# Performance work log

Hardware: AMD Instinct MI355X
Metric: run time of the kernel (lower is better)

Reference implementation:

```python
import jax, jax.numpy as jnp
import numpy as np

MAX_K = 16
CLUSTER_ITERS = 3
TEMP = 0.8
EPS = 1e-6


def setup_inputs() -> dict:
    key = jax.random.key(0)
    k1, k2 = jax.random.split(key, 2)
    B, C, H, W = 4, 256, 128, 128
    embeddings = jax.random.normal(k1, (B, C, H, W), dtype=jnp.float32)
    # 1x1 conv == per-pixel linear: weight [max_k, C], bias [max_k]
    seed_w = jax.random.normal(k2, (MAX_K, C), dtype=jnp.float32) * 0.05
    seed_b = jnp.zeros((MAX_K,), dtype=jnp.float32)
    return {"embeddings": embeddings, "seed_w": seed_w, "seed_b": seed_b, "k": 8}


def reference(embeddings, seed_w, seed_b, k):
    b, c, h, w = embeddings.shape
    n = h * w
    feats = embeddings.reshape(b, c, n)                     # [b,c,n]

    # seed_proj (1x1 conv) restricted to first k output channels
    seeds = jnp.einsum('oc,bcn->bon', seed_w[:k], feats) + seed_b[:k][None, :, None]
    assign = jax.nn.softmax(seeds, axis=1)                  # [b,k,n]
    proto = jnp.einsum('bkn,bcn->bkc', assign, feats) / (assign.sum(axis=2)[..., None] + EPS)

    # ||f||^2 is constant across iterations
    f_sq = jnp.sum(feats * feats, axis=1)                   # [b,n]

    logits = None
    for _ in range(CLUSTER_ITERS):                          # small fixed iter count
        p_sq = jnp.sum(proto * proto, axis=2)               # [b,k]
        cross = jnp.einsum('bkc,bcn->bkn', proto, feats)    # [b,k,n]
        # squared L2 distance via matmul trick (same math as (f-p)^2 sum over c)
        dist = f_sq[:, None, :] + p_sq[:, :, None] - 2.0 * cross
        logits = -dist / TEMP                               # [b,k,n]
        assign = jax.nn.softmax(logits, axis=1)
        denom = assign.sum(axis=2, keepdims=True) + EPS     # [b,k,1]
        proto = jnp.einsum('bkn,bcn->bkc', assign, feats) / denom

    logits_map = logits.reshape(b, k, h, w)
    probs = jax.nn.softmax(logits_map, axis=1)
    # bilinear upsample x4, align_corners=False (half-pixel) == jax 'linear' resize
    probs_full = jax.image.resize(probs, (b, k, 4 * h, 4 * w), method='linear')
    return probs_full, proto, logits_map
```

## Files before the change

### kernel.cpp

```cpp
#include <hip/hip_runtime.h>
#include <hip/hip_bf16.h>
#include <math.h>

#define BB   4
#define CCH  256
#define KK   8
#define NPIX 16384
#define TILE 64
#define NBLK 256
#define TEMP_INV 1.25f
#define EPSF 1e-6f

__device__ __forceinline__ float bf_lo(unsigned int u) { return __uint_as_float(u << 16); }
__device__ __forceinline__ float bf_hi(unsigned int u) { return __uint_as_float(u & 0xffff0000u); }

template<int MODE>
__global__ __launch_bounds__(512, 6)
void skm_pass(const float* __restrict__ feats,
              const float* __restrict__ seed_w,
              const float* __restrict__ seed_b,
              const float* __restrict__ proto_t,
              const float* __restrict__ psq_part,
              float* __restrict__ fsq,
              float* __restrict__ part_num,
              float* __restrict__ part_den,
              float* __restrict__ logits_out,
              float* __restrict__ probs_out)
{
    __shared__ unsigned int fb_s[CCH][32];
    __shared__ float cross_s[8][KK][66];
    __shared__ float w_s[KK][68];
    __shared__ float aux_s[8][TILE];

    const int t   = threadIdx.x;
    const int bid = blockIdx.x;
    const int b   = bid >> 8;
    const int blk = bid & 255;
    const int n0  = blk * TILE;

    const int p  = t & 63;
    const int g  = t >> 6;
    const int c0 = __builtin_amdgcn_readfirstlane(g) * 32;
    const float* fcol = feats + (size_t)b * CCH * NPIX + (size_t)c0 * NPIX + n0 + p;
    const float* pt   = proto_t + (size_t)b * CCH * KK + (size_t)c0 * KK;

    float cr[KK];
    #pragma unroll
    for (int k = 0; k < KK; ++k) cr[k] = 0.f;
    float fs = 0.f;

    #pragma unroll 8
    for (int cc = 0; cc < 32; ++cc) {
        const float f = fcol[(size_t)cc * NPIX];
        if (MODE == 0) fs = fmaf(f, f, fs);
        const int c  = c0 + cc;
        const int wp = (p >> 1) ^ ((c & 15) << 1);
        ((__hip_bfloat16*)fb_s)[(c << 6) + (wp << 1) + (p & 1)] = __float2bfloat16(f);
        if (MODE == 0) {
            #pragma unroll
            for (int k = 0; k < KK; ++k)
                cr[k] = fmaf(seed_w[k * CCH + c], f, cr[k]);
        } else {
            const float* pr = pt + cc * KK;
            #pragma unroll
            for (int k = 0; k < KK; ++k)
                cr[k] = fmaf(pr[k], f, cr[k]);
        }
    }
    #pragma unroll
    for (int k = 0; k < KK; ++k) cross_s[g][k][p] = cr[k];
    if (MODE == 0) aux_s[g][p] = fs;
    __syncthreads();

    {
        const int pp = t >> 3, k = t & 7;
        float lg = 0.f;
        #pragma unroll
        for (int gg = 0; gg < 8; ++gg) lg += cross_s[gg][k][pp];
        if (MODE == 0) {
            lg += seed_b[k];
            if (k == 0) {
                float fv = 0.f;
                #pragma unroll
                for (int gg = 0; gg < 8; ++gg) fv += aux_s[gg][pp];
                fsq[b * NPIX + n0 + pp] = fv;
            }
        } else {
            const float fv = fsq[b * NPIX + n0 + pp];
            const float4 q0 = ((const float4*)psq_part)[(b * KK + k) * 2];
            const float4 q1 = ((const float4*)psq_part)[(b * KK + k) * 2 + 1];
            const float pk = ((q0.x + q0.y) + (q0.z + q0.w))
                           + ((q1.x + q1.y) + (q1.z + q1.w));
            lg = (2.f * lg - fv - pk) * TEMP_INV;
        }
        float m = lg;
        m = fmaxf(m, __shfl_xor(m, 1, 64));
        m = fmaxf(m, __shfl_xor(m, 2, 64));
        m = fmaxf(m, __shfl_xor(m, 4, 64));
        const float e = expf(lg - m);
        float ssum = e;
        ssum += __shfl_xor(ssum, 1, 64);
        ssum += __shfl_xor(ssum, 2, 64);
        ssum += __shfl_xor(ssum, 4, 64);
        const float wv = e / ssum;
        w_s[k][pp] = wv;
        if (MODE == 2) aux_s[k][pp] = lg;
    }
    __syncthreads();

    if (MODE == 2) {
        const int k2 = t >> 6, p2 = t & 63;
        logits_out[((size_t)b * KK + k2) * NPIX + n0 + p2] = aux_s[k2][p2];
        probs_out [((size_t)b * KK + k2) * NPIX + n0 + p2] = w_s[k2][p2];
    }

    if (t < 256) {
        const int kk = t >> 5, ll = t & 31;
        float s = w_s[kk][2 * ll] + w_s[kk][2 * ll + 1];
        s += __shfl_xor(s, 16, 64);
        s += __shfl_xor(s, 8, 64);
        s += __shfl_xor(s, 4, 64);
        s += __shfl_xor(s, 2, 64);
        s += __shfl_xor(s, 1, 64);
        if (ll == 0) part_den[(b * NBLK + blk) * KK + kk] = s;
    }

    {
        const int c = t & 255, h = t >> 8;
        const int s2 = (c & 15) << 1;
        const uint2* row2 = (const uint2*)fb_s[c];
        float acc[KK];
        #pragma unroll
        for (int k = 0; k < KK; ++k) acc[k] = 0.f;
        #pragma unroll
        for (int j = 0; j < 8; ++j) {
            const uint2 u = row2[((16 * h + 2 * j) ^ s2) >> 1];
            const float f0 = bf_lo(u.x), f1 = bf_hi(u.x);
            const float f2 = bf_lo(u.y), f3 = bf_hi(u.y);
            const int px = 32 * h + 4 * j;
            #pragma unroll
            for (int k = 0; k < KK; ++k) {
                const float4 w4 = *(const float4*)&w_s[k][px];
                acc[k] = fmaf(f3, w4.w, fmaf(f2, w4.z,
                         fmaf(f1, w4.y, fmaf(f0, w4.x, acc[k]))));
            }
        }
        float (*acc_s)[KK][CCH] = (float (*)[KK][CCH])cross_s;
        #pragma unroll
        for (int k = 0; k < KK; ++k) acc_s[h][k][c] = acc[k];
        __syncthreads();
        #pragma unroll
        for (int u2 = t; u2 < KK * CCH; u2 += 512) {
            const int k = u2 >> 8, c2 = u2 & 255;
            part_num[(((size_t)b * NBLK + blk) * KK + k) * CCH + c2] =
                acc_s[0][k][c2] + acc_s[1][k][c2];
        }
    }
}

template<bool FINAL>
__global__ __launch_bounds__(256)
void skm_reduce(const float* __restrict__ part_num,
                const float* __restrict__ part_den,
                float* __restrict__ proto_t,
                float* __restrict__ psq_part,
                float* __restrict__ proto_out,
                const float* __restrict__ probs_ws,
                float* __restrict__ probs_full)
{
    const int bid = blockIdx.x;
    if (FINAL && bid >= 256) {
        const int gid = (bid - 256) * 256 + threadIdx.x;
        const int jb = gid & 127;
        const int i  = (gid >> 7) & 511;
        const int bk = gid >> 16;
        const float* src = probs_ws + (size_t)bk * NPIX;
        const float y   = i * 0.25f - 0.375f;
        const float y0f = floorf(y);
        const float fy  = y - y0f;
        const int   y0  = (int)y0f;
        const int ya = min(max(y0, 0), 127);
        const int yb = min(max(y0 + 1, 0), 127);
        const int xm = max(jb - 1, 0);
        const int xp = min(jb + 1, 127);
        const float* r0 = src + ya * 128;
        const float* r1 = src + yb * 128;
        const float wy0 = 1.f - fy;
        const float am = r0[xm] * wy0 + r1[xm] * fy;
        const float ac = r0[jb] * wy0 + r1[jb] * fy;
        const float ap = r0[xp] * wy0 + r1[xp] * fy;
        float4 o;
        o.x = 0.375f * am + 0.625f * ac;
        o.y = 0.125f * am + 0.875f * ac;
        o.z = 0.875f * ac + 0.125f * ap;
        o.w = 0.625f * ac + 0.375f * ap;
        ((float4*)probs_full)[gid] = o;
        return;
    }

    const int cq = bid & 7;
    const int bk = bid >> 3;
    const int b = bk >> 3, k = bk & 7;
    const int t = threadIdx.x;

    __shared__ float red[8][32];
    __shared__ float den_s[4];

    float dv = part_den[(b * NBLK + t) * KK + k];
    dv += __shfl_xor(dv, 32, 64);
    dv += __shfl_xor(dv, 16, 64);
    dv += __shfl_xor(dv, 8, 64);
    dv += __shfl_xor(dv, 4, 64);
    dv += __shfl_xor(dv, 2, 64);
    dv += __shfl_xor(dv, 1, 64);
    if ((t & 63) == 0) den_s[t >> 6] = dv;

    const int jj = t >> 5, cl = t & 31;
    const int c = cq * 32 + cl;
    float s = 0.f;
    #pragma unroll 4
    for (int j = 0; j < 32; ++j)
        s += part_num[(((size_t)b * NBLK + jj * 32 + j) * KK + k) * CCH + c];
    red[jj][cl] = s;
    __syncthreads();

    if (t < 32) {
        const float den = den_s[0] + den_s[1] + den_s[2] + den_s[3] + EPSF;
        float pv = 0.f;
        #pragma unroll
        for (int j2 = 0; j2 < 8; ++j2) pv += red[j2][t];
        pv /= den;
        const int c2 = cq * 32 + t;
        proto_t[((size_t)b * CCH + c2) * KK + k] = pv;
        if (proto_out) proto_out[(b * KK + k) * CCH + c2] = pv;
        float q = pv * pv;
        q += __shfl_xor(q, 16, 64);
        q += __shfl_xor(q, 8, 64);
        q += __shfl_xor(q, 4, 64);
        q += __shfl_xor(q, 2, 64);
        q += __shfl_xor(q, 1, 64);
        if (t == 0) psq_part[(b * KK + k) * 8 + cq] = q;
    }
}

extern "C" void kernel_launch(void* const* d_in, const int* in_sizes, int n_in,
                              void* d_out, int out_size, void* d_ws, size_t ws_size,
                              hipStream_t stream)
{
    const float* feats  = (const float*)d_in[0];
    const float* seed_w = (const float*)d_in[1];
    const float* seed_b = (const float*)d_in[2];

    float* out        = (float*)d_out;
    float* probs_full = out;
    float* proto_out  = out + 8388608;
    float* logits_out = out + 8388608 + 8192;

    float* ws       = (float*)d_ws;
    float* fsq      = ws;
    float* part_den = ws + 65536;
    float* proto_t  = part_den + 8192;
    float* psq_part = proto_t + 8192;
    float* probs_ws = psq_part + 256;
    float* part_num = probs_ws + 524288;

    const dim3 pg(BB * NBLK), pb(512);
    const dim3 rg(256), rb(256);

    skm_pass<0><<<pg, pb, 0, stream>>>(feats, seed_w, seed_b, proto_t, psq_part,
                                       fsq, part_num, part_den, nullptr, nullptr);
    skm_reduce<false><<<rg, rb, 0, stream>>>(part_num, part_den, proto_t, psq_part,
                                             nullptr, probs_ws, probs_full);
    skm_pass<1><<<pg, pb, 0, stream>>>(feats, seed_w, seed_b, proto_t, psq_part,
                                       fsq, part_num, part_den, nullptr, nullptr);
    skm_reduce<false><<<rg, rb, 0, stream>>>(part_num, part_den, proto_t, psq_part,
                                             nullptr, probs_ws, probs_full);
    skm_pass<1><<<pg, pb, 0, stream>>>(feats, seed_w, seed_b, proto_t, psq_part,
                                       fsq, part_num, part_den, nullptr, nullptr);
    skm_reduce<false><<<rg, rb, 0, stream>>>(part_num, part_den, proto_t, psq_part,
                                             nullptr, probs_ws, probs_full);
    skm_pass<2><<<pg, pb, 0, stream>>>(feats, seed_w, seed_b, proto_t, psq_part,
                                       fsq, part_num, part_den, logits_out, probs_ws);
    skm_reduce<true><<<dim3(256 + 8192), rb, 0, stream>>>(part_num, part_den, proto_t, psq_part,
                                                          proto_out, probs_ws, probs_full);
}
```

Baseline: 102.0 us.

## Cache bf16-packed features in first pass and reuse in later passes

The first pass now writes a bf16 copy of the features, two channels packed per 32-bit word, into workspace. Later passes read this packed copy instead of the fp32 input, which halves the feature bytes they load. The cost is an extra write pass of 32MB in pass 0. Later passes also compute the cross term from bf16-rounded values rather than fp32, which lowers accuracy.

```diff
diff --git a/kernel.cpp b/kernel.cpp
--- a/kernel.cpp
+++ b/kernel.cpp
@@ -13,6 +13,10 @@
 
 __device__ __forceinline__ float bf_lo(unsigned int u) { return __uint_as_float(u << 16); }
 __device__ __forceinline__ float bf_hi(unsigned int u) { return __uint_as_float(u & 0xffff0000u); }
+__device__ __forceinline__ unsigned short bfbits(float f) {
+    __hip_bfloat16 h = __float2bfloat16(f);
+    return *reinterpret_cast<unsigned short*>(&h);
+}
 
 template<int MODE>
 __global__ __launch_bounds__(512, 6)
@@ -25,7 +29,8 @@
               float* __restrict__ part_num,
               float* __restrict__ part_den,
               float* __restrict__ logits_out,
-              float* __restrict__ probs_out)
+              float* __restrict__ probs_out,
+              unsigned int* __restrict__ feats_pk)
 {
     __shared__ unsigned int fb_s[CCH][32];
     __shared__ float cross_s[8][KK][66];
@@ -41,35 +46,56 @@
     const int p  = t & 63;
     const int g  = t >> 6;
     const int c0 = __builtin_amdgcn_readfirstlane(g) * 32;
-    const float* fcol = feats + (size_t)b * CCH * NPIX + (size_t)c0 * NPIX + n0 + p;
-    const float* pt   = proto_t + (size_t)b * CCH * KK + (size_t)c0 * KK;
+    const float* pt = proto_t + (size_t)b * CCH * KK + (size_t)c0 * KK;
 
     float cr[KK];
     #pragma unroll
     for (int k = 0; k < KK; ++k) cr[k] = 0.f;
-    float fs = 0.f;
-
-    #pragma unroll 8
-    for (int cc = 0; cc < 32; ++cc) {
-        const float f = fcol[(size_t)cc * NPIX];
-        if (MODE == 0) fs = fmaf(f, f, fs);
-        const int c  = c0 + cc;
-        const int wp = (p >> 1) ^ ((c & 15) << 1);
-        ((__hip_bfloat16*)fb_s)[(c << 6) + (wp << 1) + (p & 1)] = __float2bfloat16(f);
-        if (MODE == 0) {
+
+    if (MODE == 0) {
+        const float* fcol = feats + (size_t)b * CCH * NPIX + (size_t)c0 * NPIX + n0 + p;
+        unsigned int* pkcol = feats_pk + (size_t)(b * 128 + (c0 >> 1)) * NPIX + n0 + p;
+        float fs = 0.f;
+        unsigned int pkbuf = 0;
+        #pragma unroll 8
+        for (int cc = 0; cc < 32; ++cc) {
+            const float f = fcol[(size_t)cc * NPIX];
+            fs = fmaf(f, f, fs);
+            const int c  = c0 + cc;
+            const int wp = (p >> 1) ^ ((c & 15) << 1);
+            const unsigned short hb = bfbits(f);
+            ((unsigned short*)fb_s)[(c << 6) + (wp << 1) + (p & 1)] = hb;
+            if ((cc & 1) == 0) pkbuf = hb;
+            else pkcol[(size_t)(cc >> 1) * NPIX] = pkbuf | ((unsigned int)hb << 16);
             #pragma unroll
             for (int k = 0; k < KK; ++k)
                 cr[k] = fmaf(seed_w[k * CCH + c], f, cr[k]);
-        } else {
-            const float* pr = pt + cc * KK;
+        }
+        aux_s[g][p] = fs;
+    } else {
+        const unsigned int* pkcol = feats_pk + (size_t)(b * 128 + (c0 >> 1)) * NPIX + n0 + p;
+        #pragma unroll 8
+        for (int j = 0; j < 16; ++j) {
+            const unsigned int u = pkcol[(size_t)j * NPIX];
+            const float f0 = bf_lo(u), f1 = bf_hi(u);
+            const int c  = c0 + 2 * j;
+            const int w0 = (p >> 1) ^ ((c & 15) << 1);
+            const int w1 = (p >> 1) ^ (((c + 1) & 15) << 1);
+            ((unsigned short*)fb_s)[(c << 6) + (w0 << 1) + (p & 1)] =
+                (unsigned short)(u & 0xffffu);
+            ((unsigned short*)fb_s)[((c + 1) << 6) + (w1 << 1) + (p & 1)] =
+                (unsigned short)(u >> 16);
+            const float* pr = pt + 2 * j * KK;
             #pragma unroll
             for (int k = 0; k < KK; ++k)
-                cr[k] = fmaf(pr[k], f, cr[k]);
+                cr[k] = fmaf(pr[k], f0, cr[k]);
+            #pragma unroll
+            for (int k = 0; k < KK; ++k)
+                cr[k] = fmaf(pr[KK + k], f1, cr[k]);
         }
     }
     #pragma unroll
     for (int k = 0; k < KK; ++k) cross_s[g][k][p] = cr[k];
-    if (MODE == 0) aux_s[g][p] = fs;
     __syncthreads();
 
     {
@@ -263,24 +289,25 @@
     float* psq_part = proto_t + 8192;
     float* probs_ws = psq_part + 256;
     float* part_num = probs_ws + 524288;
+    unsigned int* feats_pk = (unsigned int*)(part_num + 2097152);
 
     const dim3 pg(BB * NBLK), pb(512);
     const dim3 rg(256), rb(256);
 
     skm_pass<0><<<pg, pb, 0, stream>>>(feats, seed_w, seed_b, proto_t, psq_part,
-                                       fsq, part_num, part_den, nullptr, nullptr);
+                                       fsq, part_num, part_den, nullptr, nullptr, feats_pk);
     skm_reduce<false><<<rg, rb, 0, stream>>>(part_num, part_den, proto_t, psq_part,
                                              nullptr, probs_ws, probs_full);
     skm_pass<1><<<pg, pb, 0, stream>>>(feats, seed_w, seed_b, proto_t, psq_part,
-                                       fsq, part_num, part_den, nullptr, nullptr);
+                                       fsq, part_num, part_den, nullptr, nullptr, feats_pk);
     skm_reduce<false><<<rg, rb, 0, stream>>>(part_num, part_den, proto_t, psq_part,
                                              nullptr, probs_ws, probs_full);
     skm_pass<1><<<pg, pb, 0, stream>>>(feats, seed_w, seed_b, proto_t, psq_part,
-                                       fsq, part_num, part_den, nullptr, nullptr);
+                                       fsq, part_num, part_den, nullptr, nullptr, feats_pk);
     skm_reduce<false><<<rg, rb, 0, stream>>>(part_num, part_den, proto_t, psq_part,
                                              nullptr, probs_ws, probs_full);
     skm_pass<2><<<pg, pb, 0, stream>>>(feats, seed_w, seed_b, proto_t, psq_part,
-                                       fsq, part_num, part_den, logits_out, probs_ws);
+                                       fsq, part_num, part_den, logits_out, probs_ws, feats_pk);
     skm_reduce<true><<<dim3(256 + 8192), rb, 0, stream>>>(part_num, part_den, proto_t, psq_part,
                                                           proto_out, probs_ws, probs_full);
 }
```

Measured after the change: 112.9 us. 1.11x slower.
